# Kernel tuning notes

Hardware: AMD Instinct MI355X
Metric: run time of the kernel (lower is better)

The kernel has to match this reference:

```python
import jax, jax.numpy as jnp
import numpy as np

D_MODEL = 1024

def setup_inputs() -> dict:
    key = jax.random.key(0)
    k1, k2 = jax.random.split(key, 2)
    x = jax.random.normal(k1, (4, 2048, D_MODEL), dtype=jnp.float32)
    W_attn = jax.random.normal(k2, (3 * D_MODEL, D_MODEL), dtype=jnp.float32) * (1.0 / np.sqrt(D_MODEL))
    b_attn = jnp.zeros((3 * D_MODEL,), dtype=jnp.float32)
    return {"x": x, "W_attn": W_attn, "b_attn": b_attn}

def reference(x, W_attn, b_attn):
    B, T, C = x.shape
    # fused QKV projection; torch split order is (k, q, v)
    kqv = x @ W_attn.T + b_attn            # [B, T, 3C]
    k, q, v = jnp.split(kqv, 3, axis=-1)   # each [B, T, C]
    # NOTE: original computes k @ q^T (quirk), scaled by sqrt(d_model)
    scores = jnp.einsum('btc,bsc->bts', k, q) / jnp.sqrt(jnp.asarray(C, x.dtype))
    causal = jnp.tril(jnp.ones((T, T), dtype=bool))
    scores = jnp.where(causal[None, :, :], scores, -jnp.inf)
    attn = jax.nn.softmax(scores, axis=-1)
    return jnp.einsum('bts,bsc->btc', attn, v)
```

## Files before the change

### kernel.cpp

```cpp
#include <hip/hip_runtime.h>

typedef __bf16 bf16x8 __attribute__((ext_vector_type(8)));
typedef float f32x4 __attribute__((ext_vector_type(4)));
typedef float fl4 __attribute__((ext_vector_type(4)));
typedef unsigned short us4 __attribute__((ext_vector_type(4)));
typedef unsigned short us8 __attribute__((ext_vector_type(8)));

__device__ __forceinline__ unsigned short f2bf(float f) {
  unsigned u = __builtin_bit_cast(unsigned, f);
  u += 0x7fffu + ((u >> 16) & 1u);
  return (unsigned short)(u >> 16);
}
__device__ __forceinline__ float bf2f(unsigned short h) {
  unsigned u = ((unsigned)h) << 16;
  return __builtin_bit_cast(float, u);
}

__device__ __forceinline__ void async16(const void* g, void* l) {
  __builtin_amdgcn_global_load_lds(
      (const __attribute__((address_space(1))) unsigned int*)g,
      (__attribute__((address_space(3))) unsigned int*)l, 16, 0, 0);
}

#define BARM() asm volatile("s_barrier" ::: "memory")
#define VMCNT4() asm volatile("s_waitcnt vmcnt(4)" ::: "memory")
#define VMCNT6() asm volatile("s_waitcnt vmcnt(6)" ::: "memory")
#define LGKM0() asm volatile("s_waitcnt lgkmcnt(0)" ::: "memory")
#define LGKM8() asm volatile("s_waitcnt lgkmcnt(8)" ::: "memory")
#define SCHEDB() __builtin_amdgcn_sched_barrier(0)

__global__ __launch_bounds__(256) void cvt_bf16_2(const float* __restrict__ sA,
                                                  unsigned short* __restrict__ dA, int nA,
                                                  const float* __restrict__ sB,
                                                  unsigned short* __restrict__ dB, int nB) {
  int i = blockIdx.x * 256 + threadIdx.x;
  const float* s;
  unsigned short* d;
  if (i < nA) {
    s = sA; d = dA;
  } else {
    i -= nA;
    if (i >= nB) return;
    s = sB; d = dB;
  }
  fl4 f = ((const fl4*)s)[i];
  us4 o;
  o[0] = f2bf(f[0]); o[1] = f2bf(f[1]); o[2] = f2bf(f[2]); o[3] = f2bf(f[3]);
  ((us4*)d)[i] = o;
}

__global__ __launch_bounds__(256) void transpose_v(const unsigned short* __restrict__ kqv,
                                                   unsigned short* __restrict__ vT) {
  int b = blockIdx.z;
  int t0 = blockIdx.x * 64;
  int c0 = blockIdx.y * 64;
  __shared__ unsigned short tile[64][68];
  int tid = threadIdx.x;
#pragma unroll
  for (int i = 0; i < 4; ++i) {
    int idx = i * 256 + tid;
    int r = idx >> 4;
    int c4 = (idx & 15) * 4;
    const unsigned short* src = kqv + ((size_t)(b * 2048 + t0 + r)) * 3072 + 2048 + c0 + c4;
    us4 v = *(const us4*)src;
    *(us4*)&tile[r][c4] = v;
  }
  __syncthreads();
#pragma unroll
  for (int i = 0; i < 4; ++i) {
    int idx = i * 256 + tid;
    int rc = idx >> 4;
    int t4 = (idx & 15) * 4;
    us4 v;
    v[0] = tile[t4 + 0][rc]; v[1] = tile[t4 + 1][rc];
    v[2] = tile[t4 + 2][rc]; v[3] = tile[t4 + 3][rc];
    unsigned short* dst = vT + ((size_t)(b * 1024 + c0 + rc)) * 2048 + t0 + t4;
    *(us4*)dst = v;
  }
}

__global__ __launch_bounds__(512, 2) void gemm_g0(
    const unsigned short* __restrict__ A, const unsigned short* __restrict__ B,
    unsigned short* __restrict__ C, const float* __restrict__ bias) {
  const int flat = blockIdx.x;
  const int swz = (flat & 7) * 64 + (flat >> 3);
  const int bx = swz & 7;
  const int by = swz >> 3;
  const int rowBase = by * 128, colBase = bx * 384;
  const int lda = 1024, ldc = 3072, nk = 16;

  __shared__ __align__(16) unsigned char lds[131072];
  const int tid = threadIdx.x;
  const int lane = tid & 63, wid = tid >> 6;
  const int wr = wid >> 2, wc = wid & 3;
  const int l15 = lane & 15, l4 = lane >> 4, l7 = lane & 7;

  f32x4 acc[4][6] = {};
  bf16x8 af01[2][2], af23[2][2], bf[6][2];

  const unsigned short* Ab = A + (size_t)rowBase * lda;
  const unsigned short* Bb = B + (size_t)colBase * lda;
  unsigned aoff[2], boff[6], aldso[2], bldso[6];
#pragma unroll
  for (int i = 0; i < 6; ++i) {
    int off = i * 8192 + tid * 16;
    int r = off >> 7;
    int sb = ((off >> 4) & 7) ^ (r & 7);
    if (i < 2) { aoff[i] = (unsigned)(r * lda + sb * 8); aldso[i] = (unsigned)off; }
    boff[i] = (unsigned)(r * lda + sb * 8);
    bldso[i] = (unsigned)off;
  }

  auto STA = [&](int bufc, int op, int koff) {
    async16(Ab + (size_t)(aoff[op] + (unsigned)koff), lds + bufc * 65536 + aldso[op]);
  };
  auto STB = [&](int bufc, int op, int koff) {
    async16(Bb + (size_t)(boff[op] + (unsigned)koff),
            lds + bufc * 65536 + 16384 + bldso[op]);
  };
  auto RA = [&](int bufc, int m, int kk) -> bf16x8 {
    int row = wr * 64 + m * 16 + l15;
    int blk = (kk * 4 + l4) ^ l7;
    return *(const bf16x8*)(lds + bufc * 65536 + row * 128 + blk * 16);
  };
  auto RB = [&](int bufc, int n, int kk) -> bf16x8 {
    int row = wc * 96 + n * 16 + l15;
    int blk = (kk * 4 + l4) ^ l7;
    return *(const bf16x8*)(lds + bufc * 65536 + 16384 + row * 128 + blk * 16);
  };

#define RD_A01(BUF)                                                            \
  _Pragma("unroll") for (int mi = 0; mi < 2; ++mi)                             \
  _Pragma("unroll") for (int kk = 0; kk < 2; ++kk) af01[mi][kk] = RA((BUF), mi, kk)
#define RD_A23(BUF)                                                            \
  _Pragma("unroll") for (int mi = 0; mi < 2; ++mi)                             \
  _Pragma("unroll") for (int kk = 0; kk < 2; ++kk) af23[mi][kk] = RA((BUF), 2 + mi, kk)
#define RD_B(BUF, N0)                                                          \
  _Pragma("unroll") for (int nj = 0; nj < 3; ++nj)                             \
  _Pragma("unroll") for (int kk = 0; kk < 2; ++kk) bf[(N0) + nj][kk] = RB((BUF), (N0) + nj, kk)

#define MQ(MB, NB, AF)                                                         \
  _Pragma("unroll") for (int kk = 0; kk < 2; ++kk)                             \
  _Pragma("unroll") for (int mi = 0; mi < 2; ++mi)                             \
  _Pragma("unroll") for (int nj = 0; nj < 3; ++nj)                             \
      acc[(MB) + mi][(NB) + nj] = __builtin_amdgcn_mfma_f32_16x16x32_bf16(     \
          AF[mi][kk], bf[(NB) + nj][kk], acc[(MB) + mi][(NB) + nj], 0, 0, 0)

#define PHASE(RDS, STG, GATE, MB, NB, AF)                                      \
  do {                                                                         \
    RDS;                                                                       \
    STG;                                                                       \
    BARM();                                                                    \
    LGKM0();                                                                   \
    SCHEDB();                                                                  \
    __builtin_amdgcn_s_setprio(1);                                             \
    MQ(MB, NB, AF);                                                            \
    __builtin_amdgcn_s_setprio(0);                                             \
    GATE;                                                                      \
    BARM();                                                                    \
  } while (0)

  STA(0, 0, 0); STA(0, 1, 0);
#pragma unroll
  for (int i = 0; i < 6; ++i) STB(0, i, 0);
#pragma unroll
  for (int i = 0; i < 6; ++i) STB(1, i, 64);
  VMCNT6();
  BARM();

  for (int it = 0; it < 8; ++it) {
    int t = it * 2;
    int kA1 = (t + 1) * 64;
    int k2 = (t + 2 < nk - 1 ? t + 2 : nk - 1) * 64;
    int k3 = (t + 3 < nk - 1 ? t + 3 : nk - 1) * 64;
    PHASE({ RD_A01(0); RD_B(0, 0); }, { STA(1, 0, kA1); STA(1, 1, kA1); },
          (void)0, 0, 0, af01);
    PHASE({ RD_A23(0); RD_B(0, 3); }, (void)0, (void)0, 0, 3, af01);
    PHASE({}, { STB(0, 0, k2); STB(0, 1, k2); STB(0, 2, k2); },
          (void)0, 2, 3, af23);
    PHASE({}, { STB(0, 3, k2); STB(0, 4, k2); STB(0, 5, k2); },
          VMCNT6(), 2, 0, af23);
    PHASE({ RD_A01(1); RD_B(1, 0); }, { STA(0, 0, k2); STA(0, 1, k2); },
          (void)0, 0, 0, af01);
    PHASE({ RD_A23(1); RD_B(1, 3); }, (void)0, (void)0, 0, 3, af01);
    PHASE({}, { STB(1, 0, k3); STB(1, 1, k3); STB(1, 2, k3); },
          (void)0, 2, 3, af23);
    PHASE({}, { STB(1, 3, k3); STB(1, 4, k3); STB(1, 5, k3); },
          VMCNT6(), 2, 0, af23);
  }
#undef PHASE
#undef MQ
#undef RD_A01
#undef RD_A23
#undef RD_B

  const int cr = l4 * 4;
#pragma unroll
  for (int n = 0; n < 6; ++n) {
    int col = colBase + wc * 96 + n * 16 + l15;
    float bv = bias[col];
#pragma unroll
    for (int m = 0; m < 4; ++m) {
      int row = rowBase + wr * 64 + m * 16 + cr;
#pragma unroll
      for (int i = 0; i < 4; ++i)
        C[(size_t)(row + i) * ldc + col] = f2bf(acc[m][n][i] + bv);
    }
  }
}

__global__ __launch_bounds__(512, 2) void gemm_s(
    const unsigned short* __restrict__ A, int lda, long long sA,
    const unsigned short* __restrict__ B, int ldb, long long sB,
    unsigned short* __restrict__ C, int ldc, long long sC,
    float scale, int K) {
  int bx = blockIdx.x, by = blockIdx.y;
  const int bz = blockIdx.z;
  if (bx > by) return;
  A += (size_t)bz * sA;
  B += (size_t)bz * sB;
  const int rowBase = by * 256;
  const int colBase = bx * 256;
  const int nk = K / 64;

  __shared__ __align__(16) unsigned char lds[131072];
  const int tid = threadIdx.x;
  const int lane = tid & 63;
  const int wid = tid >> 6;
  const int wr = wid >> 2;
  const int wc = wid & 3;
  const int l15 = lane & 15, l4 = lane >> 4, l7 = lane & 7;

  f32x4 acc[8][4] = {};
  bf16x8 af0[4][2], af1[4][2], bf0[2][2], bf1[2][2];

  const unsigned short* Ab = A + (size_t)rowBase * lda;
  const unsigned short* Bb = B + (size_t)colBase * ldb;
  unsigned loff[2][2];
  unsigned lldso[2];
#pragma unroll
  for (int i = 0; i < 2; ++i) {
    int off = (i * 512 + tid) * 16;
    int r = off >> 7;
    int sb = ((off >> 4) & 7) ^ (r & 7);
    lldso[i] = (unsigned)off;
#pragma unroll
    for (int hh = 0; hh < 2; ++hh)
      loff[hh][i] = (unsigned)((hh * 128 + r) * lda + sb * 8);
  }

  auto STAGE = [&](int bufc, int isB, int half, const unsigned short* Gb, int koff) {
#pragma unroll
    for (int i = 0; i < 2; ++i)
      async16(Gb + (size_t)(loff[half][i] + (unsigned)koff),
              lds + bufc * 65536 + isB * 32768 + half * 16384 + lldso[i]);
  };
  auto RDA = [&](int bufc, int m, int kk) -> bf16x8 {
    int row = m * 16 + l15;
    int blk = (kk * 4 + l4) ^ l7;
    return *(const bf16x8*)(lds + bufc * 65536 + wr * 16384 + row * 128 + blk * 16);
  };
  auto RDB = [&](int bufc, int n, int kk) -> bf16x8 {
    int row = (wc & 1) * 64 + n * 16 + l15;
    int blk = (kk * 4 + l4) ^ l7;
    return *(const bf16x8*)(lds + bufc * 65536 + 32768 + (wc >> 1) * 16384 +
                            row * 128 + blk * 16);
  };

#define RDA8(dst, BUF, Q)                                                      \
  _Pragma("unroll") for (int mi = 0; mi < 4; ++mi)                             \
  _Pragma("unroll") for (int kk = 0; kk < 2; ++kk)                             \
      dst[mi][kk] = RDA((BUF), (Q) * 4 + mi, kk)
#define RDB4(dst, BUF, NB)                                                     \
  _Pragma("unroll") for (int nj = 0; nj < 2; ++nj)                             \
  _Pragma("unroll") for (int kk = 0; kk < 2; ++kk)                             \
      dst[nj][kk] = RDB((BUF), (NB) + nj, kk)

#define MFMAQ(MB, NB, AF, BF)                                                  \
  _Pragma("unroll") for (int kk = 0; kk < 2; ++kk)                             \
  _Pragma("unroll") for (int mi = 0; mi < 4; ++mi)                             \
  _Pragma("unroll") for (int nj = 0; nj < 2; ++nj)                             \
      acc[(MB) + mi][(NB) + nj] = __builtin_amdgcn_mfma_f32_16x16x32_bf16(     \
          AF[mi][kk], BF[nj][kk], acc[(MB) + mi][(NB) + nj], 0, 0, 0)

#define PH(RDS, STG, HINT, GATE, MB, NB, AF, BF)                               \
  do {                                                                         \
    RDS;                                                                       \
    STG;                                                                       \
    HINT;                                                                      \
    BARM();                                                                    \
    LGKM0();                                                                   \
    SCHEDB();                                                                  \
    __builtin_amdgcn_s_setprio(1);                                             \
    MFMAQ(MB, NB, AF, BF);                                                     \
    __builtin_amdgcn_s_setprio(0);                                             \
    GATE;                                                                      \
    BARM();                                                                    \
  } while (0)

  STAGE(0, 0, 0, Ab, 0);
  STAGE(0, 0, 1, Ab, 0);
  STAGE(0, 1, 0, Bb, 0);
  STAGE(0, 1, 1, Bb, 0);
  STAGE(1, 1, 0, Bb, 64);
  STAGE(1, 1, 1, Bb, 64);
  VMCNT4();
  BARM();

  const int nt2 = nk >> 1;
  for (int it = 0; it < nt2; ++it) {
    int t = it * 2;
    int kA1 = (t + 1) * 64;
    int k2 = (t + 2 < nk - 1 ? t + 2 : nk - 1) * 64;
    int k3 = (t + 3 < nk - 1 ? t + 3 : nk - 1) * 64;
    PH({ RDA8(af0, 0, 0); RDB4(bf0, 0, 0); }, STAGE(1, 0, 0, Ab, kA1), LGKM8(),
       (void)0, 0, 0, af0, bf0);
    PH({ RDB4(bf1, 0, 2); }, STAGE(1, 0, 1, Ab, kA1), (void)0,
       (void)0, 0, 2, af0, bf1);
    PH({ RDA8(af1, 0, 1); }, STAGE(0, 1, 0, Bb, k2), (void)0,
       (void)0, 4, 2, af1, bf1);
    PH({}, STAGE(0, 1, 1, Bb, k2), (void)0,
       VMCNT4(), 4, 0, af1, bf0);
    PH({ RDA8(af0, 1, 0); RDB4(bf0, 1, 0); }, STAGE(0, 0, 0, Ab, k2), LGKM8(),
       (void)0, 0, 0, af0, bf0);
    PH({ RDB4(bf1, 1, 2); }, STAGE(0, 0, 1, Ab, k2), (void)0,
       (void)0, 0, 2, af0, bf1);
    PH({ RDA8(af1, 1, 1); }, STAGE(1, 1, 0, Bb, k3), (void)0,
       (void)0, 4, 2, af1, bf1);
    PH({}, STAGE(1, 1, 1, Bb, k3), (void)0,
       VMCNT4(), 4, 0, af1, bf0);
  }
#undef PH
#undef MFMAQ
#undef RDA8
#undef RDB4

  const int cr = l4 * 4;
  unsigned short* Cb = C + (size_t)bz * sC;
#pragma unroll
  for (int n = 0; n < 4; ++n) {
    int col = colBase + wc * 64 + n * 16 + l15;
#pragma unroll
    for (int m = 0; m < 8; ++m) {
      int row = rowBase + wr * 128 + m * 16 + cr;
#pragma unroll
      for (int i = 0; i < 4; ++i)
        Cb[(size_t)(row + i) * ldc + col] = f2bf(acc[m][n][i] * scale);
    }
  }
}

__global__ __launch_bounds__(256, 2) void gemm_pv(
    const unsigned short* __restrict__ S, const unsigned short* __restrict__ V,
    float* __restrict__ O) {
  const int bx = blockIdx.x;
  const int by = 15 - (int)blockIdx.y;
  const int bz = blockIdx.z;
  const unsigned short* A = S + (size_t)bz * 2048 * 2048 + (size_t)(by * 128) * 2048;
  const unsigned short* B = V + (size_t)bz * 1024 * 2048 + (size_t)(bx * 128) * 2048;
  float* Ob = O + (size_t)bz * 2048 * 1024;
  const int nk = (by + 1) * 2;

  __shared__ __align__(16) unsigned char lds[32768];
  const int tid = threadIdx.x;
  const int lane = tid & 63, wid = tid >> 6;
  const int wr = (wid >> 1) * 64, wc = (wid & 1) * 64;
  const int l15 = lane & 15, l4 = lane >> 4, l7 = lane & 7;

  f32x4 acc[4][4] = {};

  unsigned goff[4], ldso[4];
#pragma unroll
  for (int i = 0; i < 4; ++i) {
    int off = (i * 256 + tid) * 16;
    int r = off >> 7;
    int sb = ((off >> 4) & 7) ^ (r & 7);
    goff[i] = (unsigned)(r * 2048 + sb * 8);
    ldso[i] = (unsigned)off;
  }

  for (int kt = 0; kt < nk; ++kt) {
    const unsigned kof = (unsigned)(kt * 64);
    __syncthreads();
#pragma unroll
    for (int i = 0; i < 4; ++i) {
      async16(A + (size_t)(goff[i] + kof), lds + ldso[i]);
      async16(B + (size_t)(goff[i] + kof), lds + 16384 + ldso[i]);
    }
    __syncthreads();
    bf16x8 af[4][2], bfr[4][2];
#pragma unroll
    for (int m = 0; m < 4; ++m) {
      int row = wr + m * 16 + l15;
#pragma unroll
      for (int kk = 0; kk < 2; ++kk)
        af[m][kk] = *(const bf16x8*)(lds + row * 128 + (((kk * 4 + l4) ^ l7) * 16));
    }
#pragma unroll
    for (int n = 0; n < 4; ++n) {
      int row = wc + n * 16 + l15;
#pragma unroll
      for (int kk = 0; kk < 2; ++kk)
        bfr[n][kk] = *(const bf16x8*)(lds + 16384 + row * 128 + (((kk * 4 + l4) ^ l7) * 16));
    }
#pragma unroll
    for (int kk = 0; kk < 2; ++kk)
#pragma unroll
      for (int m = 0; m < 4; ++m)
#pragma unroll
        for (int n = 0; n < 4; ++n)
          acc[m][n] = __builtin_amdgcn_mfma_f32_16x16x32_bf16(af[m][kk], bfr[n][kk],
                                                              acc[m][n], 0, 0, 0);
  }

  const int cr = l4 * 4;
#pragma unroll
  for (int n = 0; n < 4; ++n) {
    int col = bx * 128 + wc + n * 16 + l15;
#pragma unroll
    for (int m = 0; m < 4; ++m) {
      int row = by * 128 + wr + m * 16 + cr;
#pragma unroll
      for (int i = 0; i < 4; ++i)
        Ob[(size_t)(row + i) * 1024 + col] = acc[m][n][i];
    }
  }
}

__global__ __launch_bounds__(256) void softmax_causal(unsigned short* __restrict__ S) {
  const int T = 2048;
  int t = blockIdx.x, b = blockIdx.y;
  unsigned short* row = S + ((size_t)b * T + t) * T;
  const int nv = t + 1;
  const int bound = ((t >> 7) + 1) << 7;
  int tid = threadIdx.x;
  int lane = tid & 63, wid = tid >> 6;
  int s0 = tid * 8;
  us8 raw = {};
  if (s0 < nv) raw = *(const us8*)(row + s0);
  float v[8];
  float m = -3.0e38f;
#pragma unroll
  for (int j = 0; j < 8; ++j) {
    v[j] = bf2f(raw[j]);
    if (s0 + j < nv) m = fmaxf(m, v[j]);
  }
#pragma unroll
  for (int o = 32; o > 0; o >>= 1) m = fmaxf(m, __shfl_xor(m, o, 64));
  __shared__ float red[4];
  if (lane == 0) red[wid] = m;
  __syncthreads();
  m = fmaxf(fmaxf(red[0], red[1]), fmaxf(red[2], red[3]));
  __syncthreads();
  float sum = 0.f;
#pragma unroll
  for (int j = 0; j < 8; ++j) {
    float e = (s0 + j < nv) ? exp2f(v[j] - m) : 0.f;
    v[j] = e;
    sum += e;
  }
#pragma unroll
  for (int o = 32; o > 0; o >>= 1) sum += __shfl_xor(sum, o, 64);
  if (lane == 0) red[wid] = sum;
  __syncthreads();
  sum = red[0] + red[1] + red[2] + red[3];
  float inv = 1.0f / sum;
  if (s0 < bound) {
    us8 outv;
#pragma unroll
    for (int j = 0; j < 8; ++j) outv[j] = f2bf(v[j] * inv);
    *(us8*)(row + s0) = outv;
  }
}

extern "C" void kernel_launch(void* const* d_in, const int* in_sizes, int n_in,
                              void* d_out, int out_size, void* d_ws, size_t ws_size,
                              hipStream_t stream) {
  const float* x = (const float*)d_in[0];
  const float* W = (const float*)d_in[1];
  const float* bias = (const float*)d_in[2];
  float* out = (float*)d_out;

  char* ws = (char*)d_ws;
  if (ws_size < 106954752u) return;
  unsigned short* xbf = (unsigned short*)(ws);
  unsigned short* vT = xbf;
  unsigned short* wbf = (unsigned short*)(ws + 16777216);
  unsigned short* kqv = (unsigned short*)(ws + 23068672);
  unsigned short* S = (unsigned short*)(ws + 73400320);

  const float kSoftmaxScale = 1.4426950408889634f / 32.0f;

  cvt_bf16_2<<<11264, 256, 0, stream>>>(x, xbf, 2097152, W, wbf, 786432);

  gemm_g0<<<dim3(512, 1, 1), 512, 0, stream>>>(xbf, wbf, kqv, bias);

  transpose_v<<<dim3(32, 16, 4), 256, 0, stream>>>(kqv, vT);

  gemm_s<<<dim3(8, 8, 4), 512, 0, stream>>>(
      kqv, 3072, 2048LL * 3072, kqv + 1024, 3072, 2048LL * 3072,
      S, 2048, 2048LL * 2048, kSoftmaxScale, 1024);

  softmax_causal<<<dim3(2048, 4), 256, 0, stream>>>(S);

  gemm_pv<<<dim3(8, 16, 4), 256, 0, stream>>>(S, vT, out);
}
```

Baseline: 171.3 us.

## Fuse V transpose into scores GEMM launch and flatten PV grid ordering

Merges the V-transpose kernel into the QK^T score GEMM launch as extra blocks of one flat grid, so the transpose fills compute units idle from skipped upper-triangle tiles and one launch is removed. The transpose blocks now use 512 threads and the 128KB LDS allocation, which may reduce their occupancy. Separately, the PV GEMM grid is flattened so heavy (late-row) tiles are scheduled first, followed by light tiles, to improve load balance across the causal triangle.

```diff
diff --git a/kernel.cpp b/kernel.cpp
--- a/kernel.cpp
+++ b/kernel.cpp
@@ -47,36 +47,6 @@
   us4 o;
   o[0] = f2bf(f[0]); o[1] = f2bf(f[1]); o[2] = f2bf(f[2]); o[3] = f2bf(f[3]);
   ((us4*)d)[i] = o;
-}
-
-__global__ __launch_bounds__(256) void transpose_v(const unsigned short* __restrict__ kqv,
-                                                   unsigned short* __restrict__ vT) {
-  int b = blockIdx.z;
-  int t0 = blockIdx.x * 64;
-  int c0 = blockIdx.y * 64;
-  __shared__ unsigned short tile[64][68];
-  int tid = threadIdx.x;
-#pragma unroll
-  for (int i = 0; i < 4; ++i) {
-    int idx = i * 256 + tid;
-    int r = idx >> 4;
-    int c4 = (idx & 15) * 4;
-    const unsigned short* src = kqv + ((size_t)(b * 2048 + t0 + r)) * 3072 + 2048 + c0 + c4;
-    us4 v = *(const us4*)src;
-    *(us4*)&tile[r][c4] = v;
-  }
-  __syncthreads();
-#pragma unroll
-  for (int i = 0; i < 4; ++i) {
-    int idx = i * 256 + tid;
-    int rc = idx >> 4;
-    int t4 = (idx & 15) * 4;
-    us4 v;
-    v[0] = tile[t4 + 0][rc]; v[1] = tile[t4 + 1][rc];
-    v[2] = tile[t4 + 2][rc]; v[3] = tile[t4 + 3][rc];
-    unsigned short* dst = vT + ((size_t)(b * 1024 + c0 + rc)) * 2048 + t0 + t4;
-    *(us4*)dst = v;
-  }
 }
 
 __global__ __launch_bounds__(512, 2) void gemm_g0(
@@ -209,22 +179,57 @@
   }
 }
 
-__global__ __launch_bounds__(512, 2) void gemm_s(
-    const unsigned short* __restrict__ A, int lda, long long sA,
-    const unsigned short* __restrict__ B, int ldb, long long sB,
-    unsigned short* __restrict__ C, int ldc, long long sC,
-    float scale, int K) {
-  int bx = blockIdx.x, by = blockIdx.y;
-  const int bz = blockIdx.z;
+__global__ __launch_bounds__(512, 2) void g1_fused(
+    const unsigned short* __restrict__ kqv, unsigned short* __restrict__ S,
+    unsigned short* __restrict__ vT, float scale) {
+  __shared__ __align__(16) unsigned char lds[131072];
+  const int f = blockIdx.x;
+  const int tid = threadIdx.x;
+
+  if (f >= 256) {
+    int i = f - 256;
+    int bz = i >> 9;
+    int r = i & 511;
+    int t0 = (r >> 4) * 64;
+    int c0 = (r & 15) * 64;
+    unsigned short* tile = (unsigned short*)lds;
+#pragma unroll
+    for (int it = 0; it < 2; ++it) {
+      int idx = it * 512 + tid;
+      int rr = idx >> 4;
+      int c4 = (idx & 15) * 4;
+      const unsigned short* src =
+          kqv + ((size_t)(bz * 2048 + t0 + rr)) * 3072 + 2048 + c0 + c4;
+      us4 v = *(const us4*)src;
+      *(us4*)&tile[rr * 68 + c4] = v;
+    }
+    __syncthreads();
+#pragma unroll
+    for (int it = 0; it < 2; ++it) {
+      int idx = it * 512 + tid;
+      int rc = idx >> 4;
+      int t4 = (idx & 15) * 4;
+      us4 v;
+      v[0] = tile[(t4 + 0) * 68 + rc]; v[1] = tile[(t4 + 1) * 68 + rc];
+      v[2] = tile[(t4 + 2) * 68 + rc]; v[3] = tile[(t4 + 3) * 68 + rc];
+      unsigned short* dst = vT + ((size_t)(bz * 1024 + c0 + rc)) * 2048 + t0 + t4;
+      *(us4*)dst = v;
+    }
+    return;
+  }
+
+  const int bz = f >> 6;
+  const int rr = f & 63;
+  const int bx = rr & 7;
+  const int by = rr >> 3;
   if (bx > by) return;
-  A += (size_t)bz * sA;
-  B += (size_t)bz * sB;
+  const unsigned short* A = kqv + (size_t)bz * 2048 * 3072;
+  const unsigned short* B = A + 1024;
+  const int lda = 3072;
   const int rowBase = by * 256;
   const int colBase = bx * 256;
-  const int nk = K / 64;
-
-  __shared__ __align__(16) unsigned char lds[131072];
-  const int tid = threadIdx.x;
+  const int nk = 16;
+
   const int lane = tid & 63;
   const int wid = tid >> 6;
   const int wr = wid >> 2;
@@ -235,7 +240,7 @@
   bf16x8 af0[4][2], af1[4][2], bf0[2][2], bf1[2][2];
 
   const unsigned short* Ab = A + (size_t)rowBase * lda;
-  const unsigned short* Bb = B + (size_t)colBase * ldb;
+  const unsigned short* Bb = B + (size_t)colBase * lda;
   unsigned loff[2][2];
   unsigned lldso[2];
 #pragma unroll
@@ -336,7 +341,7 @@
 #undef RDB4
 
   const int cr = l4 * 4;
-  unsigned short* Cb = C + (size_t)bz * sC;
+  unsigned short* Cb = S + (size_t)bz * 2048 * 2048;
 #pragma unroll
   for (int n = 0; n < 4; ++n) {
     int col = colBase + wc * 64 + n * 16 + l15;
@@ -345,7 +350,7 @@
       int row = rowBase + wr * 128 + m * 16 + cr;
 #pragma unroll
       for (int i = 0; i < 4; ++i)
-        Cb[(size_t)(row + i) * ldc + col] = f2bf(acc[m][n][i] * scale);
+        Cb[(size_t)(row + i) * 2048 + col] = f2bf(acc[m][n][i] * scale);
     }
   }
 }
@@ -353,9 +358,14 @@
 __global__ __launch_bounds__(256, 2) void gemm_pv(
     const unsigned short* __restrict__ S, const unsigned short* __restrict__ V,
     float* __restrict__ O) {
-  const int bx = blockIdx.x;
-  const int by = 15 - (int)blockIdx.y;
-  const int bz = blockIdx.z;
+  const int f = blockIdx.x;
+  const int halfsel = f >> 8;
+  const int i = f & 255;
+  const int bz = i >> 6;
+  const int r = i & 63;
+  const int bx = r & 7;
+  const int p = r >> 3;
+  const int by = halfsel ? p : (15 - p);
   const unsigned short* A = S + (size_t)bz * 2048 * 2048 + (size_t)(by * 128) * 2048;
   const unsigned short* B = V + (size_t)bz * 1024 * 2048 + (size_t)(bx * 128) * 2048;
   float* Ob = O + (size_t)bz * 2048 * 1024;
@@ -371,21 +381,21 @@
 
   unsigned goff[4], ldso[4];
 #pragma unroll
-  for (int i = 0; i < 4; ++i) {
-    int off = (i * 256 + tid) * 16;
-    int r = off >> 7;
-    int sb = ((off >> 4) & 7) ^ (r & 7);
-    goff[i] = (unsigned)(r * 2048 + sb * 8);
-    ldso[i] = (unsigned)off;
+  for (int ii = 0; ii < 4; ++ii) {
+    int off = (ii * 256 + tid) * 16;
+    int rr = off >> 7;
+    int sb = ((off >> 4) & 7) ^ (rr & 7);
+    goff[ii] = (unsigned)(rr * 2048 + sb * 8);
+    ldso[ii] = (unsigned)off;
   }
 
   for (int kt = 0; kt < nk; ++kt) {
     const unsigned kof = (unsigned)(kt * 64);
     __syncthreads();
 #pragma unroll
-    for (int i = 0; i < 4; ++i) {
-      async16(A + (size_t)(goff[i] + kof), lds + ldso[i]);
-      async16(B + (size_t)(goff[i] + kof), lds + 16384 + ldso[i]);
+    for (int ii = 0; ii < 4; ++ii) {
+      async16(A + (size_t)(goff[ii] + kof), lds + ldso[ii]);
+      async16(B + (size_t)(goff[ii] + kof), lds + 16384 + ldso[ii]);
     }
     __syncthreads();
     bf16x8 af[4][2], bfr[4][2];
@@ -421,8 +431,8 @@
     for (int m = 0; m < 4; ++m) {
       int row = by * 128 + wr + m * 16 + cr;
 #pragma unroll
-      for (int i = 0; i < 4; ++i)
-        Ob[(size_t)(row + i) * 1024 + col] = acc[m][n][i];
+      for (int i2 = 0; i2 < 4; ++i2)
+        Ob[(size_t)(row + i2) * 1024 + col] = acc[m][n][i2];
     }
   }
 }
@@ -495,13 +505,9 @@
 
   gemm_g0<<<dim3(512, 1, 1), 512, 0, stream>>>(xbf, wbf, kqv, bias);
 
-  transpose_v<<<dim3(32, 16, 4), 256, 0, stream>>>(kqv, vT);
-
-  gemm_s<<<dim3(8, 8, 4), 512, 0, stream>>>(
-      kqv, 3072, 2048LL * 3072, kqv + 1024, 3072, 2048LL * 3072,
-      S, 2048, 2048LL * 2048, kSoftmaxScale, 1024);
+  g1_fused<<<dim3(2304, 1, 1), 512, 0, stream>>>(kqv, S, vT, kSoftmaxScale);
 
   softmax_causal<<<dim3(2048, 4), 256, 0, stream>>>(S);
 
-  gemm_pv<<<dim3(8, 16, 4), 256, 0, stream>>>(S, vT, out);
-}
+  gemm_pv<<<dim3(512, 1, 1), 256, 0, stream>>>(S, vT, out);
+}
```

Result: no change. 170.7 us (-0.4%).

## Pair causal row tiles per block and double-buffer PV GEMM loads

Applied to the files above, without the earlier changes.

The P·V GEMM now gives each block two row tiles, a long one (15-p) and a short one (p). This balances causal triangular work and cuts the launch to 256 equal-work blocks. It adds double-buffered LDS with async global-to-LDS loads issued ahead of the MFMA work, plus a raised wave priority during MFMA. The cost is double the LDS (64KB) and two accumulator sets, which raises register pressure and may reduce occupancy.

```diff
diff --git a/kernel.cpp b/kernel.cpp
--- a/kernel.cpp
+++ b/kernel.cpp
@@ -25,6 +25,7 @@
 #define BARM() asm volatile("s_barrier" ::: "memory")
 #define VMCNT4() asm volatile("s_waitcnt vmcnt(4)" ::: "memory")
 #define VMCNT6() asm volatile("s_waitcnt vmcnt(6)" ::: "memory")
+#define VMCNT8() asm volatile("s_waitcnt vmcnt(8)" ::: "memory")
 #define LGKM0() asm volatile("s_waitcnt lgkmcnt(0)" ::: "memory")
 #define LGKM8() asm volatile("s_waitcnt lgkmcnt(8)" ::: "memory")
 #define SCHEDB() __builtin_amdgcn_sched_barrier(0)
@@ -350,68 +351,106 @@
   }
 }
 
-__global__ __launch_bounds__(256, 2) void gemm_pv(
+__global__ __launch_bounds__(256, 2) void gemm_pv2(
     const unsigned short* __restrict__ S, const unsigned short* __restrict__ V,
     float* __restrict__ O) {
-  const int bx = blockIdx.x;
-  const int by = 15 - (int)blockIdx.y;
-  const int bz = blockIdx.z;
-  const unsigned short* A = S + (size_t)bz * 2048 * 2048 + (size_t)(by * 128) * 2048;
-  const unsigned short* B = V + (size_t)bz * 1024 * 2048 + (size_t)(bx * 128) * 2048;
+  const int f = blockIdx.x;
+  const int bx = f & 7;
+  const int p = (f >> 3) & 7;
+  const int bz = f >> 6;
+  const int byH = 15 - p;
+  const int nkL = 2 * (p + 1);
+  const int nkH = 32 - 2 * p;
+  const unsigned short* base = S + (size_t)bz * 2048 * 2048;
+  const unsigned short* AH = base + (size_t)(byH * 128) * 2048;
+  const unsigned short* AL = base + (size_t)(p * 128) * 2048;
+  const unsigned short* Bb = V + (size_t)bz * 1024 * 2048 + (size_t)(bx * 128) * 2048;
   float* Ob = O + (size_t)bz * 2048 * 1024;
-  const int nk = (by + 1) * 2;
-
-  __shared__ __align__(16) unsigned char lds[32768];
+
+  __shared__ __align__(16) unsigned char lds[65536];
   const int tid = threadIdx.x;
   const int lane = tid & 63, wid = tid >> 6;
   const int wr = (wid >> 1) * 64, wc = (wid & 1) * 64;
   const int l15 = lane & 15, l4 = lane >> 4, l7 = lane & 7;
 
-  f32x4 acc[4][4] = {};
+  f32x4 accH[4][4] = {}, accL[4][4] = {};
 
   unsigned goff[4], ldso[4];
 #pragma unroll
-  for (int i = 0; i < 4; ++i) {
-    int off = (i * 256 + tid) * 16;
-    int r = off >> 7;
-    int sb = ((off >> 4) & 7) ^ (r & 7);
-    goff[i] = (unsigned)(r * 2048 + sb * 8);
-    ldso[i] = (unsigned)off;
-  }
-
-  for (int kt = 0; kt < nk; ++kt) {
-    const unsigned kof = (unsigned)(kt * 64);
-    __syncthreads();
-#pragma unroll
-    for (int i = 0; i < 4; ++i) {
-      async16(A + (size_t)(goff[i] + kof), lds + ldso[i]);
-      async16(B + (size_t)(goff[i] + kof), lds + 16384 + ldso[i]);
+  for (int ii = 0; ii < 4; ++ii) {
+    int off = (ii * 256 + tid) * 16;
+    int rr = off >> 7;
+    int sb = ((off >> 4) & 7) ^ (rr & 7);
+    goff[ii] = (unsigned)(rr * 2048 + sb * 8);
+    ldso[ii] = (unsigned)off;
+  }
+
+  auto ST = [&](int buf, const unsigned short* Ap, unsigned kof) {
+#pragma unroll
+    for (int ii = 0; ii < 4; ++ii) {
+      async16(Ap + (size_t)(goff[ii] + kof), lds + buf * 32768 + ldso[ii]);
+      async16(Bb + (size_t)(goff[ii] + kof), lds + buf * 32768 + 16384 + ldso[ii]);
     }
-    __syncthreads();
-    bf16x8 af[4][2], bfr[4][2];
-#pragma unroll
-    for (int m = 0; m < 4; ++m) {
-      int row = wr + m * 16 + l15;
-#pragma unroll
-      for (int kk = 0; kk < 2; ++kk)
-        af[m][kk] = *(const bf16x8*)(lds + row * 128 + (((kk * 4 + l4) ^ l7) * 16));
+  };
+  auto ITEM = [&](int i, const unsigned short*& P, unsigned& kf) {
+    if (i < 2 * nkL) {
+      P = (i & 1) ? AL : AH;
+      kf = (unsigned)((i >> 1) * 64);
+    } else {
+      P = AH;
+      kf = (unsigned)((i - nkL) * 64);
     }
-#pragma unroll
-    for (int n = 0; n < 4; ++n) {
-      int row = wc + n * 16 + l15;
-#pragma unroll
-      for (int kk = 0; kk < 2; ++kk)
-        bfr[n][kk] = *(const bf16x8*)(lds + 16384 + row * 128 + (((kk * 4 + l4) ^ l7) * 16));
-    }
-#pragma unroll
-    for (int kk = 0; kk < 2; ++kk)
-#pragma unroll
-      for (int m = 0; m < 4; ++m)
-#pragma unroll
-        for (int n = 0; n < 4; ++n)
-          acc[m][n] = __builtin_amdgcn_mfma_f32_16x16x32_bf16(af[m][kk], bfr[n][kk],
-                                                              acc[m][n], 0, 0, 0);
-  }
+  };
+
+#define PVSTEP(BUF, ACC, NITEM)                                                \
+  do {                                                                         \
+    const unsigned short* nP;                                                  \
+    unsigned nK;                                                               \
+    ITEM((NITEM) < 33 ? (NITEM) : 33, nP, nK);                                 \
+    VMCNT8();                                                                  \
+    BARM();                                                                    \
+    bf16x8 af[4][2], bfr[4][2];                                                \
+    _Pragma("unroll") for (int m = 0; m < 4; ++m) {                            \
+      int row = wr + m * 16 + l15;                                             \
+      _Pragma("unroll") for (int kk = 0; kk < 2; ++kk)                         \
+        af[m][kk] = *(const bf16x8*)(lds + (BUF) * 32768 + row * 128 +         \
+                                     (((kk * 4 + l4) ^ l7) * 16));             \
+    }                                                                          \
+    _Pragma("unroll") for (int n = 0; n < 4; ++n) {                            \
+      int row = wc + n * 16 + l15;                                             \
+      _Pragma("unroll") for (int kk = 0; kk < 2; ++kk)                         \
+        bfr[n][kk] = *(const bf16x8*)(lds + (BUF) * 32768 + 16384 + row * 128 +\
+                                      (((kk * 4 + l4) ^ l7) * 16));            \
+    }                                                                          \
+    LGKM0();                                                                   \
+    BARM();                                                                    \
+    ST((BUF), nP, nK);                                                         \
+    SCHEDB();                                                                  \
+    __builtin_amdgcn_s_setprio(1);                                             \
+    _Pragma("unroll") for (int kk = 0; kk < 2; ++kk)                           \
+    _Pragma("unroll") for (int m = 0; m < 4; ++m)                              \
+    _Pragma("unroll") for (int n = 0; n < 4; ++n)                              \
+      ACC[m][n] = __builtin_amdgcn_mfma_f32_16x16x32_bf16(af[m][kk], bfr[n][kk],\
+                                                          ACC[m][n], 0, 0, 0); \
+    __builtin_amdgcn_s_setprio(0);                                             \
+  } while (0)
+
+  ST(0, AH, 0);
+  {
+    const unsigned short* P; unsigned kf;
+    ITEM(1, P, kf);
+    ST(1, P, kf);
+  }
+
+  for (int t = 0; t < nkL; ++t) {
+    PVSTEP(0, accH, 2 * t + 2);
+    PVSTEP(1, accL, 2 * t + 3);
+  }
+  for (int u = nkL; u < nkH; u += 2) {
+    PVSTEP(0, accH, u + nkL + 2);
+    PVSTEP(1, accH, u + nkL + 3);
+  }
+#undef PVSTEP
 
   const int cr = l4 * 4;
 #pragma unroll
@@ -419,10 +458,13 @@
     int col = bx * 128 + wc + n * 16 + l15;
 #pragma unroll
     for (int m = 0; m < 4; ++m) {
-      int row = by * 128 + wr + m * 16 + cr;
-#pragma unroll
-      for (int i = 0; i < 4; ++i)
-        Ob[(size_t)(row + i) * 1024 + col] = acc[m][n][i];
+      int rH = byH * 128 + wr + m * 16 + cr;
+      int rL = p * 128 + wr + m * 16 + cr;
+#pragma unroll
+      for (int i = 0; i < 4; ++i) {
+        Ob[(size_t)(rH + i) * 1024 + col] = accH[m][n][i];
+        Ob[(size_t)(rL + i) * 1024 + col] = accL[m][n][i];
+      }
     }
   }
 }
@@ -503,5 +545,5 @@
 
   softmax_causal<<<dim3(2048, 4), 256, 0, stream>>>(S);
 
-  gemm_pv<<<dim3(8, 16, 4), 256, 0, stream>>>(S, vT, out);
-}
+  gemm_pv2<<<dim3(256, 1, 1), 256, 0, stream>>>(S, vT, out);
+}
```

Result: faster. 167.6 us, median of 2 (-2.2%).
